# Optimization experiments

Measured on AMD Instinct MI355X. Metric: run time of the kernel, lower is better.

Reference implementation:

```python
import jax, jax.numpy as jnp
import numpy as np

N, B, S, E, D, L, H, OUT = 16384, 32, 512, 262144, 256, 4, 4, 768
DH = D // H
ATOM_VOCABS = [119, 9, 12, 12, 10, 6, 9, 2, 2]
BOND_VOCABS = [22, 6, 2]
BN_EPS = 1e-5


def bn(x, g, b):
    # BatchNorm1d over nodes (training-mode statistics, deterministic)
    mu = x.mean(0)
    var = ((x - mu) ** 2).mean(0)
    return (x - mu) * jax.lax.rsqrt(var + BN_EPS) * g + b


def setup_inputs():
    key = jax.random.key(0)
    ks = iter(jax.random.split(key, 80))
    x = jnp.stack([jax.random.randint(next(ks), (N,), 0, v) for v in ATOM_VOCABS], 1)
    edge_attr = jnp.stack([jax.random.randint(next(ks), (E,), 0, v) for v in BOND_VOCABS], 1)
    epg = E // B  # edges per graph, edges stay within their graph
    gid = jnp.arange(E) // epg
    src = jax.random.randint(next(ks), (E,), 0, S) + gid * S
    dst = jax.random.randint(next(ks), (E,), 0, S) + gid * S
    edge_index = jnp.stack([src, dst], 0)
    batch_vec = jnp.arange(N) // S  # B equal-sized graphs, contiguous

    def rn(shape, std=0.02):
        return jax.random.normal(next(ks), shape, jnp.float32) * std

    inp = dict(x=x, edge_attr=edge_attr, edge_index=edge_index, batch_vec=batch_vec)
    inp['atom_tab'] = rn((len(ATOM_VOCABS), max(ATOM_VOCABS), D))
    inp['bond_tab'] = rn((len(BOND_VOCABS), max(BOND_VOCABS), D))
    inp['elin_w'] = rn((L, D, D)); inp['elin_b'] = jnp.zeros((L, D))
    inp['eps'] = jnp.zeros((L,))  # GINE train_eps init 0
    inp['gw1'] = rn((L, D, 2 * D)); inp['gb1'] = jnp.zeros((L, 2 * D))
    inp['gw2'] = rn((L, 2 * D, D)); inp['gb2'] = jnp.zeros((L, D))
    inp['aw_in'] = rn((L, D, 3 * D)); inp['ab_in'] = jnp.zeros((L, 3 * D))
    inp['aw_out'] = rn((L, D, D)); inp['ab_out'] = jnp.zeros((L, D))
    for n in ('n1', 'n2', 'n3'):
        inp[n + 'g'] = jnp.ones((L, D)); inp[n + 'b'] = jnp.zeros((L, D))
    inp['mw1'] = rn((L, D, 2 * D)); inp['mb1'] = jnp.zeros((L, 2 * D))
    inp['mw2'] = rn((L, 2 * D, D)); inp['mb2'] = jnp.zeros((L, D))
    inp['pw1'] = rn((D, D)); inp['pb1'] = jnp.zeros((D,))
    inp['pw2'] = rn((D, OUT)); inp['pb2'] = jnp.zeros((OUT,))
    return inp


def forward(x, edge_attr, edge_index, batch_vec, atom_tab, bond_tab, elin_w, elin_b, eps,
            gw1, gb1, gw2, gb2, aw_in, ab_in, aw_out, ab_out,
            n1g, n1b, n2g, n2b, n3g, n3b, mw1, mb1, mw2, mb2,
            pw1, pb1, pw2, pb2):
    # AtomEncoder / BondEncoder: sum of per-feature embeddings
    h = atom_tab[jnp.arange(atom_tab.shape[0])[None, :], x].sum(1)      # [N, D]
    e = bond_tab[jnp.arange(bond_tab.shape[0])[None, :], edge_attr].sum(1)  # [E, D]
    src, dst = edge_index[0], edge_index[1]
    scale = 1.0 / np.sqrt(DH)
    for l in range(L):
        # --- GINEConv local branch ---
        el = e @ elin_w[l] + elin_b[l]                       # edge lin
        msg = jax.nn.relu(h[src] + el)                       # [E, D]
        agg = jax.ops.segment_sum(msg, dst, num_segments=N)  # scatter-add
        hc = (1.0 + eps[l]) * h + agg
        hc = jax.nn.relu(hc @ gw1[l] + gb1[l]) @ gw2[l] + gb2[l]
        hc = bn(hc + h, n1g[l], n1b[l])
        # --- global multihead attention (dense per-graph batch, all slots valid) ---
        hd = h.reshape(B, S, D)
        qkv = hd @ aw_in[l] + ab_in[l]
        q, k, v = jnp.split(qkv, 3, axis=-1)
        q = q.reshape(B, S, H, DH).transpose(0, 2, 1, 3)
        k = k.reshape(B, S, H, DH).transpose(0, 2, 1, 3)
        v = v.reshape(B, S, H, DH).transpose(0, 2, 1, 3)
        attn = jax.nn.softmax(jnp.einsum('bhqd,bhkd->bhqk', q, k) * scale, axis=-1)
        ao = jnp.einsum('bhqk,bhkd->bhqd', attn, v).transpose(0, 2, 1, 3).reshape(N, D)
        ao = ao @ aw_out[l] + ab_out[l]
        ha = bn(ao + h, n2g[l], n2b[l])
        # --- combine + MLP ---
        out = hc + ha
        out = out + (jax.nn.relu(out @ mw1[l] + mb1[l]) @ mw2[l] + mb2[l])
        h = bn(out, n3g[l], n3b[l])
    # global mean pool
    counts = jax.ops.segment_sum(jnp.ones((N, 1), h.dtype), batch_vec, num_segments=B)
    g = jax.ops.segment_sum(h, batch_vec, num_segments=B) / counts
    z = jax.nn.relu(g @ pw1 + pb1) @ pw2 + pb2
    return z / jnp.linalg.norm(z, axis=-1, keepdims=True)


def reference(x, edge_attr, edge_index, batch_vec, atom_tab, bond_tab, elin_w, elin_b, eps,
              gw1, gb1, gw2, gb2, aw_in, ab_in, aw_out, ab_out,
              n1g, n1b, n2g, n2b, n3g, n3b, mw1, mb1, mw2, mb2,
              pw1, pb1, pw2, pb2):
    return forward(x, edge_attr, edge_index, batch_vec, atom_tab, bond_tab, elin_w, elin_b, eps,
                   gw1, gb1, gw2, gb2, aw_in, ab_in, aw_out, ab_out,
                   n1g, n1b, n2g, n2b, n3g, n3b, mw1, mb1, mw2, mb2,
                   pw1, pb1, pw2, pb2)
```

## Files before the change

kernel.cpp:

```cpp
#include <hip/hip_runtime.h>
#include <hip/hip_bf16.h>
#include <math.h>

#define N_NODES 16384
#define NB      32
#define S_PG    512
#define NE      262144
#define EPG     8192
#define D       256
#define D2      512
#define D3      768
#define NL      4
#define NH      4
#define DHD     64
#define OUTD    768
#define NCOMBO  264
#define WT_PER_LAYER 786432

typedef short s8v __attribute__((ext_vector_type(8)));
typedef float f4v __attribute__((ext_vector_type(4)));

__device__ __forceinline__ unsigned bfr(float f) {
    unsigned u = __float_as_uint(f);
    return (u + 0x7fffu + ((u >> 16) & 1u)) >> 16;
}
__device__ __forceinline__ float b2f(unsigned short u) {
    return __uint_as_float(((unsigned)u) << 16);
}

__global__ __launch_bounds__(256) void k_atom_enc(const int* __restrict__ x,
                                                  const float* __restrict__ tab,
                                                  float* __restrict__ h,
                                                  unsigned short* __restrict__ hb) {
    int node = blockIdx.x * 4 + (threadIdx.x >> 6);
    int lane = threadIdx.x & 63;
    int dd = lane << 2;
    float4 acc = {0.f, 0.f, 0.f, 0.f};
#pragma unroll
    for (int f = 0; f < 9; ++f) {
        int v = x[node * 9 + f];
        const float4 t = *(const float4*)&tab[((size_t)(f * 119 + v)) * D + dd];
        acc.x += t.x; acc.y += t.y; acc.z += t.z; acc.w += t.w;
    }
    *(float4*)&h[(size_t)node * D + dd] = acc;
    ushort4 o;
    o.x = (unsigned short)bfr(acc.x); o.y = (unsigned short)bfr(acc.y);
    o.z = (unsigned short)bfr(acc.z); o.w = (unsigned short)bfr(acc.w);
    *(ushort4*)&hb[(size_t)node * D + dd] = o;
}

__global__ __launch_bounds__(256) void k_bondw(const float* __restrict__ bond_tab,
                                               const float* __restrict__ elin_w,
                                               float* __restrict__ bw) {
    int blk = blockIdx.x;
    int l = blk / 66, fv = blk % 66;
    int dout = threadIdx.x;
    const float* tabrow = bond_tab + (size_t)fv * D;
    const float* w = elin_w + (size_t)l * D * D;
    float acc = 0.f;
    for (int d = 0; d < D; ++d) acc = fmaf(tabrow[d], w[d * D + dout], acc);
    bw[((size_t)l * 66 + fv) * D + dout] = acc;
}

__global__ __launch_bounds__(256) void k_combo(const float* __restrict__ bw,
                                               const float* __restrict__ elin_b,
                                               unsigned short* __restrict__ ctb) {
    int b = blockIdx.x;
    int l = b / NCOMBO, cid = b % NCOMBO;
    int a0 = cid / 12, a1 = (cid % 12) / 2, a2 = cid & 1;
    int d = threadIdx.x;
    const float* bwl = bw + (size_t)l * 66 * D;
    float v = bwl[(size_t)a0 * D + d] + bwl[(size_t)(22 + a1) * D + d] +
              bwl[(size_t)(44 + a2) * D + d] + elin_b[(size_t)l * D + d];
    ctb[((size_t)l * NCOMBO + cid) * D + d] = (unsigned short)bfr(v);
}

__global__ __launch_bounds__(256) void k_zero16k(int* __restrict__ p) {
    p[blockIdx.x * 256 + threadIdx.x] = 0;
}
__global__ __launch_bounds__(256) void k_zero_stats(float* __restrict__ p) {
    for (int i = 0; i < 6; ++i) p[i * 256 + threadIdx.x] = 0.f;
}
__global__ __launch_bounds__(256) void k_hist(const int* __restrict__ dst, int* __restrict__ deg) {
    int e = blockIdx.x * 256 + threadIdx.x;
    atomicAdd(&deg[dst[e]], 1);
}
__global__ __launch_bounds__(256) void k_scan(const int* __restrict__ deg,
                                              int* __restrict__ row_ptr,
                                              int* __restrict__ cursor) {
    __shared__ int partial[256];
    int t = threadIdx.x;
    int base = t * 64;
    int s = 0;
    for (int i = 0; i < 64; ++i) s += deg[base + i];
    partial[t] = s;
    __syncthreads();
    for (int dstp = 1; dstp < 256; dstp <<= 1) {
        int v = (t >= dstp) ? partial[t - dstp] : 0;
        __syncthreads();
        partial[t] += v;
        __syncthreads();
    }
    int run = partial[t] - s;
    for (int i = 0; i < 64; ++i) {
        int dcur = deg[base + i];
        row_ptr[base + i] = run;
        cursor[base + i] = run;
        run += dcur;
    }
    if (t == 255) row_ptr[N_NODES] = run;
}
__global__ __launch_bounds__(256) void k_scatter(const int* __restrict__ src,
                                                 const int* __restrict__ dst,
                                                 const int* __restrict__ ea,
                                                 int* __restrict__ cursor,
                                                 int2* __restrict__ sorted) {
    int e = blockIdx.x * 256 + threadIdx.x;
    int d = dst[e];
    int pos = atomicAdd(&cursor[d], 1);
    int cid = ea[e * 3] * 12 + ea[e * 3 + 1] * 2 + ea[e * 3 + 2];
    sorted[pos] = make_int2(src[e], cid);
}

__global__ __launch_bounds__(256) void k_gine_agg(const unsigned short* __restrict__ hb,
                                                  const float* __restrict__ h,
                                                  const unsigned short* __restrict__ ctb,
                                                  const float* __restrict__ eps, int l,
                                                  const int* __restrict__ row_ptr,
                                                  const int2* __restrict__ sorted,
                                                  unsigned short* __restrict__ aggb) {
    int w = threadIdx.x >> 6;
    int lane = threadIdx.x & 63;
    int n = blockIdx.x * 4 + w;
    int dd = lane << 2;
    int beg = row_ptr[n], end = row_ptr[n + 1];
    float4 acc = {0.f, 0.f, 0.f, 0.f};
    int i = beg;
    for (; i + 2 <= end; i += 2) {
        int2 e0 = sorted[i];
        int2 e1 = sorted[i + 1];
        ushort4 h0 = *(const ushort4*)&hb[(size_t)e0.x * D + dd];
        ushort4 c0 = *(const ushort4*)&ctb[(size_t)e0.y * D + dd];
        ushort4 h1 = *(const ushort4*)&hb[(size_t)e1.x * D + dd];
        ushort4 c1 = *(const ushort4*)&ctb[(size_t)e1.y * D + dd];
        acc.x += fmaxf(b2f(h0.x) + b2f(c0.x), 0.f) + fmaxf(b2f(h1.x) + b2f(c1.x), 0.f);
        acc.y += fmaxf(b2f(h0.y) + b2f(c0.y), 0.f) + fmaxf(b2f(h1.y) + b2f(c1.y), 0.f);
        acc.z += fmaxf(b2f(h0.z) + b2f(c0.z), 0.f) + fmaxf(b2f(h1.z) + b2f(c1.z), 0.f);
        acc.w += fmaxf(b2f(h0.w) + b2f(c0.w), 0.f) + fmaxf(b2f(h1.w) + b2f(c1.w), 0.f);
    }
    if (i < end) {
        int2 e0 = sorted[i];
        ushort4 h0 = *(const ushort4*)&hb[(size_t)e0.x * D + dd];
        ushort4 c0 = *(const ushort4*)&ctb[(size_t)e0.y * D + dd];
        acc.x += fmaxf(b2f(h0.x) + b2f(c0.x), 0.f);
        acc.y += fmaxf(b2f(h0.y) + b2f(c0.y), 0.f);
        acc.z += fmaxf(b2f(h0.z) + b2f(c0.z), 0.f);
        acc.w += fmaxf(b2f(h0.w) + b2f(c0.w), 0.f);
    }
    float s1p = 1.f + eps[l];
    float4 hn = *(const float4*)&h[(size_t)n * D + dd];
    ushort4 o;
    o.x = (unsigned short)bfr(s1p * hn.x + acc.x);
    o.y = (unsigned short)bfr(s1p * hn.y + acc.y);
    o.z = (unsigned short)bfr(s1p * hn.z + acc.z);
    o.w = (unsigned short)bfr(s1p * hn.w + acc.w);
    *(ushort4*)&aggb[(size_t)n * D + dd] = o;
}

__global__ __launch_bounds__(256) void k_wcvt(const float* __restrict__ gw1, const float* __restrict__ gw2,
                                              const float* __restrict__ aw_in, const float* __restrict__ aw_out,
                                              const float* __restrict__ mw1, const float* __restrict__ mw2,
                                              unsigned short* __restrict__ WT) {
    const int KS[6]   = {256, 512, 256, 256, 256, 512};
    const int NS[6]   = {512, 256, 768, 256, 512, 256};
    const int TOFF[7] = {0, 128, 256, 448, 512, 640, 768};
    const int DOFF[6] = {0, 131072, 262144, 458752, 524288, 655360};
    int b = blockIdx.x;
    int l = b / 768, wb = b % 768;
    int widx = 0;
    while (wb >= TOFF[widx + 1]) ++widx;
    int t = wb - TOFF[widx];
    int K = KS[widx], N = NS[widx];
    int nn = N / 32;
    int kt = t / nn, nt = t % nn;
    const float* srcs[6] = {gw1, gw2, aw_in, aw_out, mw1, mw2};
    const float* W = srcs[widx] + (size_t)l * K * N;
    unsigned short* WTp = WT + (size_t)l * WT_PER_LAYER + DOFF[widx];
    __shared__ float tile[32][33];
    int tid = threadIdx.x;
    int r = tid >> 3, c4 = (tid & 7) << 2;
    float4 v = *(const float4*)&W[(size_t)(kt * 32 + r) * N + nt * 32 + c4];
    tile[r][c4] = v.x; tile[r][c4 + 1] = v.y; tile[r][c4 + 2] = v.z; tile[r][c4 + 3] = v.w;
    __syncthreads();
    int nr = tid >> 3, kc = (tid & 7) << 2;
    ushort4 o;
    o.x = (unsigned short)bfr(tile[kc + 0][nr]);
    o.y = (unsigned short)bfr(tile[kc + 1][nr]);
    o.z = (unsigned short)bfr(tile[kc + 2][nr]);
    o.w = (unsigned short)bfr(tile[kc + 3][nr]);
    *(ushort4*)&WTp[(size_t)(nt * 32 + nr) * K + kt * 32 + kc] = o;
}

template<int RELU, int RES, int OBF, int STAT>
__global__ __launch_bounds__(256) void k_mm2(const unsigned short* __restrict__ A,
                                             const unsigned short* __restrict__ BT,
                                             const float* __restrict__ bias,
                                             const float* __restrict__ res,
                                             void* __restrict__ Cp,
                                             float* __restrict__ stat,
                                             int M, int N, int K) {
    __shared__ unsigned short As[128 * 64];
    __shared__ unsigned short Bs[128 * 64];
    const int tid = threadIdx.x;
    const int row0 = blockIdx.y * 128, col0 = blockIdx.x * 128;
    const int w = tid >> 6, l = tid & 63;
    const int wm = w >> 1, wn = w & 1;
    const int lr = l & 15, lq = l >> 4;
    const int srow = l >> 3;
    const int scol = (l & 7) * 8;
    f4v acc[4][4] = {};

    const unsigned short* Ag = A + (size_t)(row0 + w * 32 + srow) * K + scol;
    const unsigned short* Bg = BT + (size_t)(col0 + w * 32 + srow) * K + scol;
    unsigned short* Al = &As[(w * 32) * 64];
    unsigned short* Bl = &Bs[(w * 32) * 64];

    for (int k0 = 0; k0 < K; k0 += 64) {
#pragma unroll
        for (int it = 0; it < 4; ++it) {
            __builtin_amdgcn_global_load_lds(
                (const __attribute__((address_space(1))) unsigned*)(Ag + (size_t)(it * 8) * K + k0),
                (__attribute__((address_space(3))) unsigned*)(Al + it * 8 * 64), 16, 0, 0);
            __builtin_amdgcn_global_load_lds(
                (const __attribute__((address_space(1))) unsigned*)(Bg + (size_t)(it * 8) * K + k0),
                (__attribute__((address_space(3))) unsigned*)(Bl + it * 8 * 64), 16, 0, 0);
        }
        asm volatile("s_waitcnt vmcnt(0)" ::: "memory");
        __syncthreads();
#pragma unroll
        for (int kk = 0; kk < 2; ++kk) {
            s8v af[4], bf[4];
#pragma unroll
            for (int m = 0; m < 4; ++m)
                af[m] = *(const s8v*)&As[(wm * 64 + m * 16 + lr) * 64 + kk * 32 + lq * 8];
#pragma unroll
            for (int n = 0; n < 4; ++n)
                bf[n] = *(const s8v*)&Bs[(wn * 64 + n * 16 + lr) * 64 + kk * 32 + lq * 8];
#pragma unroll
            for (int m = 0; m < 4; ++m)
#pragma unroll
                for (int n = 0; n < 4; ++n)
                    acc[m][n] = __builtin_amdgcn_mfma_f32_16x16x32_bf16(af[m], bf[n], acc[m][n], 0, 0, 0);
        }
        __syncthreads();
    }
    float cs[4], cs2[4];
#pragma unroll
    for (int n = 0; n < 4; ++n) { cs[n] = 0.f; cs2[n] = 0.f; }
#pragma unroll
    for (int n = 0; n < 4; ++n) {
        int c = col0 + wn * 64 + n * 16 + lr;
        float bv = bias[c];
#pragma unroll
        for (int m = 0; m < 4; ++m) {
#pragma unroll
            for (int j = 0; j < 4; ++j) {
                int r = row0 + wm * 64 + m * 16 + lq * 4 + j;
                float v = acc[m][n][j] + bv;
                if (RES) v += res[(size_t)r * N + c];
                if (STAT) { cs[n] += v; cs2[n] += v * v; }
                if (RELU) v = fmaxf(v, 0.f);
                if (OBF) ((unsigned short*)Cp)[(size_t)r * N + c] = (unsigned short)bfr(v);
                else ((float*)Cp)[(size_t)r * N + c] = v;
            }
        }
    }
    if (STAT) {
#pragma unroll
        for (int n = 0; n < 4; ++n) {
            float s = cs[n], s2 = cs2[n];
            s += __shfl_xor(s, 16);  s2 += __shfl_xor(s2, 16);
            s += __shfl_xor(s, 32);  s2 += __shfl_xor(s2, 32);
            if (lq == 0) {
                int c = col0 + wn * 64 + n * 16 + lr;
                atomicAdd(&stat[c], s);
                atomicAdd(&stat[256 + c], s2);
            }
        }
    }
}

__global__ __launch_bounds__(256) void k_bn_finish(float* __restrict__ acc,
                                                   float* __restrict__ ms) {
    int c = threadIdx.x;
    float s = acc[c], s2 = acc[256 + c];
    float mean = s / (float)N_NODES;
    float var = s2 / (float)N_NODES - mean * mean;
    ms[c] = mean;
    ms[D + c] = rsqrtf(var + 1e-5f);
    acc[c] = 0.f;
    acc[256 + c] = 0.f;
}

__global__ __launch_bounds__(256) void k_bn12(const float* __restrict__ t1,
                                              const float* __restrict__ ms1,
                                              const float* __restrict__ g1,
                                              const float* __restrict__ b1,
                                              const float* __restrict__ t2,
                                              const float* __restrict__ ms2,
                                              const float* __restrict__ g2,
                                              const float* __restrict__ b2,
                                              float* __restrict__ y,
                                              unsigned short* __restrict__ yb) {
    size_t i4 = (size_t)blockIdx.x * blockDim.x + threadIdx.x;
    int c = (int)((i4 & 63) << 2);
    float4 v1 = ((const float4*)t1)[i4];
    float4 v2 = ((const float4*)t2)[i4];
    float4 v;
    v.x = (v1.x - ms1[c + 0]) * ms1[D + c + 0] * g1[c + 0] + b1[c + 0]
        + (v2.x - ms2[c + 0]) * ms2[D + c + 0] * g2[c + 0] + b2[c + 0];
    v.y = (v1.y - ms1[c + 1]) * ms1[D + c + 1] * g1[c + 1] + b1[c + 1]
        + (v2.y - ms2[c + 1]) * ms2[D + c + 1] * g2[c + 1] + b2[c + 1];
    v.z = (v1.z - ms1[c + 2]) * ms1[D + c + 2] * g1[c + 2] + b1[c + 2]
        + (v2.z - ms2[c + 2]) * ms2[D + c + 2] * g2[c + 2] + b2[c + 2];
    v.w = (v1.w - ms1[c + 3]) * ms1[D + c + 3] * g1[c + 3] + b1[c + 3]
        + (v2.w - ms2[c + 3]) * ms2[D + c + 3] * g2[c + 3] + b2[c + 3];
    ((float4*)y)[i4] = v;
    ushort4 o;
    o.x = (unsigned short)bfr(v.x); o.y = (unsigned short)bfr(v.y);
    o.z = (unsigned short)bfr(v.z); o.w = (unsigned short)bfr(v.w);
    ((ushort4*)yb)[i4] = o;
}

__global__ __launch_bounds__(256) void k_bn_apply(const float* __restrict__ x,
                                                  const float* __restrict__ ms,
                                                  const float* __restrict__ g,
                                                  const float* __restrict__ b,
                                                  float* __restrict__ y,
                                                  unsigned short* __restrict__ yb) {
    size_t i4 = (size_t)blockIdx.x * blockDim.x + threadIdx.x;
    int c = (int)((i4 & 63) << 2);
    float4 v = ((const float4*)x)[i4];
    v.x = (v.x - ms[c + 0]) * ms[D + c + 0] * g[c + 0] + b[c + 0];
    v.y = (v.y - ms[c + 1]) * ms[D + c + 1] * g[c + 1] + b[c + 1];
    v.z = (v.z - ms[c + 2]) * ms[D + c + 2] * g[c + 2] + b[c + 2];
    v.w = (v.w - ms[c + 3]) * ms[D + c + 3] * g[c + 3] + b[c + 3];
    ((float4*)y)[i4] = v;
    ushort4 o;
    o.x = (unsigned short)bfr(v.x); o.y = (unsigned short)bfr(v.y);
    o.z = (unsigned short)bfr(v.z); o.w = (unsigned short)bfr(v.w);
    ((ushort4*)yb)[i4] = o;
}

__global__ __launch_bounds__(256) void k_flash_mfma(const unsigned short* __restrict__ qkv,
                                                    unsigned short* __restrict__ ao) {
    __shared__ unsigned short Ks[64][72];
    __shared__ unsigned short VT[64][66];
    __shared__ unsigned short Ps[4][16][72];
    const int bh = blockIdx.x;
    const int b = bh >> 2, hh = bh & 3;
    const int i0 = blockIdx.y << 6;
    const int tid = threadIdx.x;
    const int w = tid >> 6, l = tid & 63;
    const int lr = l & 15, lq = l >> 4;
    const int hd = hh * DHD;
    const size_t rowbase = (size_t)(b * S_PG) * D3;

    s8v aq[2];
    {
        const unsigned short* qrow = &qkv[rowbase + (size_t)(i0 + w * 16 + lr) * D3 + hd + lq * 8];
        aq[0] = *(const s8v*)&qrow[0];
        aq[1] = *(const s8v*)&qrow[32];
    }

    float mrow[4] = {-INFINITY, -INFINITY, -INFINITY, -INFINITY};
    float lrow[4] = {0.f, 0.f, 0.f, 0.f};
    f4v oacc[4] = {};

    const int skv = tid >> 2;
    const int sd0 = (tid & 3) << 4;

    for (int j0 = 0; j0 < S_PG; j0 += 64) {
        __syncthreads();
        {
            const unsigned short* kr = &qkv[rowbase + (size_t)(j0 + skv) * D3 + D + hd + sd0];
            *(uint4*)&Ks[skv][sd0]     = *(const uint4*)&kr[0];
            *(uint4*)&Ks[skv][sd0 + 8] = *(const uint4*)&kr[8];
            const unsigned short* vr = &qkv[rowbase + (size_t)(j0 + skv) * D3 + D2 + hd + sd0];
            unsigned short vv[16];
            *(uint4*)&vv[0] = *(const uint4*)&vr[0];
            *(uint4*)&vv[8] = *(const uint4*)&vr[8];
#pragma unroll
            for (int i = 0; i < 16; ++i) VT[sd0 + i][skv] = vv[i];
        }
        __syncthreads();
        f4v sc[4] = {};
#pragma unroll
        for (int nt = 0; nt < 4; ++nt) {
            s8v bk0 = *(const s8v*)&Ks[nt * 16 + lr][lq * 8];
            s8v bk1 = *(const s8v*)&Ks[nt * 16 + lr][32 + lq * 8];
            sc[nt] = __builtin_amdgcn_mfma_f32_16x16x32_bf16(aq[0], bk0, sc[nt], 0, 0, 0);
            sc[nt] = __builtin_amdgcn_mfma_f32_16x16x32_bf16(aq[1], bk1, sc[nt], 0, 0, 0);
        }
        float ps[4][4], alpha[4];
#pragma unroll
        for (int j = 0; j < 4; ++j) {
#pragma unroll
            for (int nt = 0; nt < 4; ++nt) ps[nt][j] = sc[nt][j] * 0.125f;
            float pm = fmaxf(fmaxf(ps[0][j], ps[1][j]), fmaxf(ps[2][j], ps[3][j]));
#pragma unroll
            for (int off = 1; off < 16; off <<= 1) pm = fmaxf(pm, __shfl_xor(pm, off));
            float mn = fmaxf(mrow[j], pm);
            alpha[j] = __expf(mrow[j] - mn);
            float rs = 0.f;
#pragma unroll
            for (int nt = 0; nt < 4; ++nt) { ps[nt][j] = __expf(ps[nt][j] - mn); rs += ps[nt][j]; }
#pragma unroll
            for (int off = 1; off < 16; off <<= 1) rs += __shfl_xor(rs, off);
            lrow[j] = lrow[j] * alpha[j] + rs;
            mrow[j] = mn;
        }
#pragma unroll
        for (int nt = 0; nt < 4; ++nt)
#pragma unroll
            for (int j = 0; j < 4; ++j)
                Ps[w][lq * 4 + j][nt * 16 + lr] = (unsigned short)bfr(ps[nt][j]);
#pragma unroll
        for (int ntd = 0; ntd < 4; ++ntd)
#pragma unroll
            for (int j = 0; j < 4; ++j) oacc[ntd][j] *= alpha[j];
        s8v pa0 = *(const s8v*)&Ps[w][lr][lq * 8];
        s8v pa1 = *(const s8v*)&Ps[w][lr][32 + lq * 8];
#pragma unroll
        for (int ntd = 0; ntd < 4; ++ntd) {
            s8v bv0 = *(const s8v*)&VT[ntd * 16 + lr][lq * 8];
            s8v bv1 = *(const s8v*)&VT[ntd * 16 + lr][32 + lq * 8];
            oacc[ntd] = __builtin_amdgcn_mfma_f32_16x16x32_bf16(pa0, bv0, oacc[ntd], 0, 0, 0);
            oacc[ntd] = __builtin_amdgcn_mfma_f32_16x16x32_bf16(pa1, bv1, oacc[ntd], 0, 0, 0);
        }
    }
#pragma unroll
    for (int j = 0; j < 4; ++j) {
        float inv = 1.f / lrow[j];
        int node = b * S_PG + i0 + w * 16 + lq * 4 + j;
#pragma unroll
        for (int ntd = 0; ntd < 4; ++ntd)
            ao[(size_t)node * D + hd + ntd * 16 + lr] = (unsigned short)bfr(oacc[ntd][j] * inv);
    }
}

__global__ __launch_bounds__(256) void k_pool(const float* __restrict__ h, float* __restrict__ g) {
    int b = blockIdx.x, c = threadIdx.x;
    const float* p = h + (size_t)b * S_PG * D + c;
    float s = 0.f;
    for (int r = 0; r < S_PG; ++r) s += p[(size_t)r * D];
    g[b * D + c] = s * (1.f / (float)S_PG);
}

__global__ __launch_bounds__(256) void k_final(const float* __restrict__ g,
                                               const float* __restrict__ pw1,
                                               const float* __restrict__ pb1,
                                               const float* __restrict__ pw2,
                                               const float* __restrict__ pb2,
                                               float* __restrict__ out) {
    __shared__ float gs[D];
    __shared__ float ts[D];
    __shared__ float red[4];
    int b = blockIdx.x, tid = threadIdx.x;
    gs[tid] = g[b * D + tid];
    __syncthreads();
    float acc = pb1[tid];
    for (int d = 0; d < D; ++d) acc = fmaf(gs[d], pw1[d * D + tid], acc);
    ts[tid] = fmaxf(acc, 0.f);
    __syncthreads();
    float z[3];
#pragma unroll
    for (int rep = 0; rep < 3; ++rep) {
        int j = tid + rep * 256;
        float a = pb2[j];
        for (int d = 0; d < D; ++d) a = fmaf(ts[d], pw2[(size_t)d * OUTD + j], a);
        z[rep] = a;
    }
    float ss = z[0] * z[0] + z[1] * z[1] + z[2] * z[2];
#pragma unroll
    for (int o = 32; o >= 1; o >>= 1) ss += __shfl_xor(ss, o);
    if ((tid & 63) == 0) red[tid >> 6] = ss;
    __syncthreads();
    float rn = rsqrtf(red[0] + red[1] + red[2] + red[3]);
#pragma unroll
    for (int rep = 0; rep < 3; ++rep) out[b * OUTD + tid + rep * 256] = z[rep] * rn;
}

extern "C" void kernel_launch(void* const* d_in, const int* in_sizes, int n_in,
                              void* d_out, int out_size, void* d_ws, size_t ws_size,
                              hipStream_t stream) {
    const int* x        = (const int*)d_in[0];
    const int* ea       = (const int*)d_in[1];
    const int* eidx     = (const int*)d_in[2];
    const float* atom_tab = (const float*)d_in[4];
    const float* bond_tab = (const float*)d_in[5];
    const float* elin_w = (const float*)d_in[6];
    const float* elin_b = (const float*)d_in[7];
    const float* eps    = (const float*)d_in[8];
    const float* gw1    = (const float*)d_in[9];
    const float* gb1    = (const float*)d_in[10];
    const float* gw2    = (const float*)d_in[11];
    const float* gb2    = (const float*)d_in[12];
    const float* aw_in  = (const float*)d_in[13];
    const float* ab_in  = (const float*)d_in[14];
    const float* aw_out = (const float*)d_in[15];
    const float* ab_out = (const float*)d_in[16];
    const float* n1g    = (const float*)d_in[17];
    const float* n1b    = (const float*)d_in[18];
    const float* n2g    = (const float*)d_in[19];
    const float* n2b    = (const float*)d_in[20];
    const float* n3g    = (const float*)d_in[21];
    const float* n3b    = (const float*)d_in[22];
    const float* mw1    = (const float*)d_in[23];
    const float* mb1    = (const float*)d_in[24];
    const float* mw2    = (const float*)d_in[25];
    const float* mb2    = (const float*)d_in[26];
    const float* pw1    = (const float*)d_in[27];
    const float* pb1    = (const float*)d_in[28];
    const float* pw2    = (const float*)d_in[29];
    const float* pb2    = (const float*)d_in[30];

    char* ws = (char*)d_ws;
    size_t off = 0;
    auto alloc = [&](size_t bytes) {
        void* p = ws + off;
        off += (bytes + 255) & ~(size_t)255;
        return p;
    };
    float*  h    = (float*)alloc((size_t)N_NODES * D * 4);
    float*  bufB = (float*)alloc((size_t)N_NODES * D * 4);
    float*  tmp1 = (float*)alloc((size_t)N_NODES * D * 4);
    unsigned short* hb = (unsigned short*)alloc((size_t)N_NODES * D * 2);
    char*   U    = (char*)alloc((size_t)N_NODES * D3 * 2);
    unsigned short* bfA = (unsigned short*)alloc((size_t)N_NODES * D3 * 2);
    unsigned short* WT  = (unsigned short*)alloc((size_t)NL * WT_PER_LAYER * 2);
    float*  bw   = (float*)alloc((size_t)NL * 66 * D * 4);
    unsigned short* ctb = (unsigned short*)alloc((size_t)NL * NCOMBO * D * 2);
    int*    deg  = (int*)alloc((size_t)N_NODES * 4);
    int*    row_ptr = (int*)alloc((size_t)(N_NODES + 1) * 4);
    int*    cursor  = (int*)alloc((size_t)N_NODES * 4);
    int2*   sorted  = (int2*)alloc((size_t)NE * 8);
    float*  statacc = (float*)alloc((size_t)3 * 512 * 4);
    float*  msbuf   = (float*)alloc((size_t)3 * 2 * D * 4);
    float*  g    = (float*)alloc((size_t)NB * D * 4);
    (void)ws_size; (void)in_sizes; (void)n_in; (void)out_size;

    float* tmp23 = (float*)U;
    unsigned short* qkv = (unsigned short*)U;
    unsigned short* aggb  = bfA;
    unsigned short* ao    = bfA;
    unsigned short* bufBb = bfA;
    unsigned short* hid   = bfA + (size_t)N_NODES * D;
    float* ms1 = msbuf, *ms2 = msbuf + 2 * D, *ms3 = msbuf + 4 * D;

    const int* srcp = eidx;
    const int* dstp = eidx + NE;
    const int EW = N_NODES * D / 1024;

    k_zero16k<<<N_NODES / 256, 256, 0, stream>>>(deg);
    k_zero_stats<<<1, 256, 0, stream>>>(statacc);
    k_hist<<<NE / 256, 256, 0, stream>>>(dstp, deg);
    k_scan<<<1, 256, 0, stream>>>(deg, row_ptr, cursor);
    k_scatter<<<NE / 256, 256, 0, stream>>>(srcp, dstp, ea, cursor, sorted);
    k_atom_enc<<<N_NODES / 4, 256, 0, stream>>>(x, atom_tab, h, hb);
    k_bondw<<<NL * 66, 256, 0, stream>>>(bond_tab, elin_w, bw);
    k_combo<<<NL * NCOMBO, 256, 0, stream>>>(bw, elin_b, ctb);
    k_wcvt<<<NL * 768, 256, 0, stream>>>(gw1, gw2, aw_in, aw_out, mw1, mw2, WT);

    for (int l = 0; l < NL; ++l) {
        const unsigned short* WTl = WT + (size_t)l * WT_PER_LAYER;
        k_gine_agg<<<N_NODES / 4, 256, 0, stream>>>(hb, h, ctb + (size_t)l * NCOMBO * D, eps, l,
                                                    row_ptr, sorted, aggb);
        k_mm2<1, 0, 1, 0><<<dim3(D2 / 128, N_NODES / 128), 256, 0, stream>>>(
            aggb, WTl + 0, gb1 + (size_t)l * D2, nullptr, hid, nullptr, N_NODES, D2, D);
        k_mm2<0, 1, 0, 1><<<dim3(D / 128, N_NODES / 128), 256, 0, stream>>>(
            hid, WTl + 131072, gb2 + (size_t)l * D, h, tmp1, statacc, N_NODES, D, D2);
        k_bn_finish<<<1, 256, 0, stream>>>(statacc, ms1);
        k_mm2<0, 0, 1, 0><<<dim3(D3 / 128, N_NODES / 128), 256, 0, stream>>>(
            hb, WTl + 262144, ab_in + (size_t)l * D3, nullptr, qkv, nullptr, N_NODES, D3, D);
        k_flash_mfma<<<dim3(NB * NH, S_PG / 64), 256, 0, stream>>>(qkv, ao);
        k_mm2<0, 1, 0, 1><<<dim3(D / 128, N_NODES / 128), 256, 0, stream>>>(
            ao, WTl + 458752, ab_out + (size_t)l * D, h, tmp23, statacc + 512, N_NODES, D, D);
        k_bn_finish<<<1, 256, 0, stream>>>(statacc + 512, ms2);
        k_bn12<<<EW, 256, 0, stream>>>(tmp1, ms1, n1g + l * D, n1b + l * D,
                                       tmp23, ms2, n2g + l * D, n2b + l * D, bufB, bufBb);
        k_mm2<1, 0, 1, 0><<<dim3(D2 / 128, N_NODES / 128), 256, 0, stream>>>(
            bufBb, WTl + 524288, mb1 + (size_t)l * D2, nullptr, hid, nullptr, N_NODES, D2, D);
        k_mm2<0, 1, 0, 1><<<dim3(D / 128, N_NODES / 128), 256, 0, stream>>>(
            hid, WTl + 655360, mb2 + (size_t)l * D, bufB, tmp23, statacc + 1024, N_NODES, D, D2);
        k_bn_finish<<<1, 256, 0, stream>>>(statacc + 1024, ms3);
        k_bn_apply<<<EW, 256, 0, stream>>>(tmp23, ms3, n3g + l * D, n3b + l * D, h, hb);
    }
    k_pool<<<NB, 256, 0, stream>>>(h, g);
    k_final<<<NB, 256, 0, stream>>>(g, pw1, pb1, pw2, pb2, (float*)d_out);
}
```

Before: 1.009 ms.

## Fuse GINE and QKV GEMMs, use 64-row tiles for narrow GEMMs, merge BN finish

New measurement: 942.9 us. 1.07x faster.

```diff
diff --git a/kernel.cpp b/kernel.cpp
--- a/kernel.cpp
+++ b/kernel.cpp
@@ -290,6 +290,171 @@
     }
 }
 
+__global__ __launch_bounds__(256) void k_mm2_dual(const unsigned short* __restrict__ A1,
+                                                  const unsigned short* __restrict__ B1,
+                                                  const float* __restrict__ bias1,
+                                                  unsigned short* __restrict__ C1, int N1, int nb1,
+                                                  const unsigned short* __restrict__ A2,
+                                                  const unsigned short* __restrict__ B2,
+                                                  const float* __restrict__ bias2,
+                                                  unsigned short* __restrict__ C2, int N2,
+                                                  int K) {
+    __shared__ unsigned short As[128 * 64];
+    __shared__ unsigned short Bs[128 * 64];
+    const unsigned short* A; const unsigned short* BT; const float* bias;
+    unsigned short* C; int N, cb, relu;
+    if ((int)blockIdx.x < nb1) { A = A1; BT = B1; bias = bias1; C = C1; N = N1; cb = blockIdx.x; relu = 1; }
+    else { A = A2; BT = B2; bias = bias2; C = C2; N = N2; cb = blockIdx.x - nb1; relu = 0; }
+    const int tid = threadIdx.x;
+    const int row0 = blockIdx.y * 128, col0 = cb * 128;
+    const int w = tid >> 6, l = tid & 63;
+    const int wm = w >> 1, wn = w & 1;
+    const int lr = l & 15, lq = l >> 4;
+    const int srow = l >> 3;
+    const int scol = (l & 7) * 8;
+    f4v acc[4][4] = {};
+
+    const unsigned short* Ag = A + (size_t)(row0 + w * 32 + srow) * K + scol;
+    const unsigned short* Bg = BT + (size_t)(col0 + w * 32 + srow) * K + scol;
+    unsigned short* Al = &As[(w * 32) * 64];
+    unsigned short* Bl = &Bs[(w * 32) * 64];
+
+    for (int k0 = 0; k0 < K; k0 += 64) {
+#pragma unroll
+        for (int it = 0; it < 4; ++it) {
+            __builtin_amdgcn_global_load_lds(
+                (const __attribute__((address_space(1))) unsigned*)(Ag + (size_t)(it * 8) * K + k0),
+                (__attribute__((address_space(3))) unsigned*)(Al + it * 8 * 64), 16, 0, 0);
+            __builtin_amdgcn_global_load_lds(
+                (const __attribute__((address_space(1))) unsigned*)(Bg + (size_t)(it * 8) * K + k0),
+                (__attribute__((address_space(3))) unsigned*)(Bl + it * 8 * 64), 16, 0, 0);
+        }
+        asm volatile("s_waitcnt vmcnt(0)" ::: "memory");
+        __syncthreads();
+#pragma unroll
+        for (int kk = 0; kk < 2; ++kk) {
+            s8v af[4], bf[4];
+#pragma unroll
+            for (int m = 0; m < 4; ++m)
+                af[m] = *(const s8v*)&As[(wm * 64 + m * 16 + lr) * 64 + kk * 32 + lq * 8];
+#pragma unroll
+            for (int n = 0; n < 4; ++n)
+                bf[n] = *(const s8v*)&Bs[(wn * 64 + n * 16 + lr) * 64 + kk * 32 + lq * 8];
+#pragma unroll
+            for (int m = 0; m < 4; ++m)
+#pragma unroll
+                for (int n = 0; n < 4; ++n)
+                    acc[m][n] = __builtin_amdgcn_mfma_f32_16x16x32_bf16(af[m], bf[n], acc[m][n], 0, 0, 0);
+        }
+        __syncthreads();
+    }
+#pragma unroll
+    for (int n = 0; n < 4; ++n) {
+        int c = col0 + wn * 64 + n * 16 + lr;
+        float bv = bias[c];
+#pragma unroll
+        for (int m = 0; m < 4; ++m) {
+#pragma unroll
+            for (int j = 0; j < 4; ++j) {
+                int r = row0 + wm * 64 + m * 16 + lq * 4 + j;
+                float v = acc[m][n][j] + bv;
+                if (relu) v = fmaxf(v, 0.f);
+                C[(size_t)r * N + c] = (unsigned short)bfr(v);
+            }
+        }
+    }
+}
+
+template<int RELU, int RES, int OBF, int STAT>
+__global__ __launch_bounds__(256) void k_mm64(const unsigned short* __restrict__ A,
+                                              const unsigned short* __restrict__ BT,
+                                              const float* __restrict__ bias,
+                                              const float* __restrict__ res,
+                                              void* __restrict__ Cp,
+                                              float* __restrict__ stat,
+                                              int M, int N, int K) {
+    __shared__ unsigned short As[64 * 64];
+    __shared__ unsigned short Bs[128 * 64];
+    const int tid = threadIdx.x;
+    const int row0 = blockIdx.y * 64, col0 = blockIdx.x * 128;
+    const int w = tid >> 6, l = tid & 63;
+    const int wn = w;
+    const int lr = l & 15, lq = l >> 4;
+    const int srow = l >> 3;
+    const int scol = (l & 7) * 8;
+    f4v acc[4][2] = {};
+
+    const unsigned short* Ag = A + (size_t)(row0 + w * 16 + srow) * K + scol;
+    const unsigned short* Bg = BT + (size_t)(col0 + w * 32 + srow) * K + scol;
+    unsigned short* Al = &As[(w * 16) * 64];
+    unsigned short* Bl = &Bs[(w * 32) * 64];
+
+    for (int k0 = 0; k0 < K; k0 += 64) {
+#pragma unroll
+        for (int it = 0; it < 2; ++it)
+            __builtin_amdgcn_global_load_lds(
+                (const __attribute__((address_space(1))) unsigned*)(Ag + (size_t)(it * 8) * K + k0),
+                (__attribute__((address_space(3))) unsigned*)(Al + it * 8 * 64), 16, 0, 0);
+#pragma unroll
+        for (int it = 0; it < 4; ++it)
+            __builtin_amdgcn_global_load_lds(
+                (const __attribute__((address_space(1))) unsigned*)(Bg + (size_t)(it * 8) * K + k0),
+                (__attribute__((address_space(3))) unsigned*)(Bl + it * 8 * 64), 16, 0, 0);
+        asm volatile("s_waitcnt vmcnt(0)" ::: "memory");
+        __syncthreads();
+#pragma unroll
+        for (int kk = 0; kk < 2; ++kk) {
+            s8v af[4], bf[2];
+#pragma unroll
+            for (int m = 0; m < 4; ++m)
+                af[m] = *(const s8v*)&As[(m * 16 + lr) * 64 + kk * 32 + lq * 8];
+#pragma unroll
+            for (int n = 0; n < 2; ++n)
+                bf[n] = *(const s8v*)&Bs[(wn * 32 + n * 16 + lr) * 64 + kk * 32 + lq * 8];
+#pragma unroll
+            for (int m = 0; m < 4; ++m)
+#pragma unroll
+                for (int n = 0; n < 2; ++n)
+                    acc[m][n] = __builtin_amdgcn_mfma_f32_16x16x32_bf16(af[m], bf[n], acc[m][n], 0, 0, 0);
+        }
+        __syncthreads();
+    }
+    float cs[2], cs2[2];
+#pragma unroll
+    for (int n = 0; n < 2; ++n) { cs[n] = 0.f; cs2[n] = 0.f; }
+#pragma unroll
+    for (int n = 0; n < 2; ++n) {
+        int c = col0 + wn * 32 + n * 16 + lr;
+        float bv = bias[c];
+#pragma unroll
+        for (int m = 0; m < 4; ++m) {
+#pragma unroll
+            for (int j = 0; j < 4; ++j) {
+                int r = row0 + m * 16 + lq * 4 + j;
+                float v = acc[m][n][j] + bv;
+                if (RES) v += res[(size_t)r * N + c];
+                if (STAT) { cs[n] += v; cs2[n] += v * v; }
+                if (RELU) v = fmaxf(v, 0.f);
+                if (OBF) ((unsigned short*)Cp)[(size_t)r * N + c] = (unsigned short)bfr(v);
+                else ((float*)Cp)[(size_t)r * N + c] = v;
+            }
+        }
+    }
+    if (STAT) {
+#pragma unroll
+        for (int n = 0; n < 2; ++n) {
+            float s = cs[n], s2 = cs2[n];
+            s += __shfl_xor(s, 16);  s2 += __shfl_xor(s2, 16);
+            s += __shfl_xor(s, 32);  s2 += __shfl_xor(s2, 32);
+            if (lq == 0) {
+                int c = col0 + wn * 32 + n * 16 + lr;
+                atomicAdd(&stat[c], s);
+                atomicAdd(&stat[256 + c], s2);
+            }
+        }
+    }
+}
+
 __global__ __launch_bounds__(256) void k_bn_finish(float* __restrict__ acc,
                                                    float* __restrict__ ms) {
     int c = threadIdx.x;
@@ -300,6 +465,20 @@
     ms[D + c] = rsqrtf(var + 1e-5f);
     acc[c] = 0.f;
     acc[256 + c] = 0.f;
+}
+__global__ __launch_bounds__(256) void k_bn_finish2(float* __restrict__ acc,
+                                                    float* __restrict__ ms) {
+    int s0 = blockIdx.x;
+    float* a = acc + (size_t)s0 * 512;
+    float* m = ms + (size_t)s0 * 2 * D;
+    int c = threadIdx.x;
+    float s = a[c], s2 = a[256 + c];
+    float mean = s / (float)N_NODES;
+    float var = s2 / (float)N_NODES - mean * mean;
+    m[c] = mean;
+    m[D + c] = rsqrtf(var + 1e-5f);
+    a[c] = 0.f;
+    a[256 + c] = 0.f;
 }
 
 __global__ __launch_bounds__(256) void k_bn12(const float* __restrict__ t1,
@@ -355,7 +534,7 @@
 __global__ __launch_bounds__(256) void k_flash_mfma(const unsigned short* __restrict__ qkv,
                                                     unsigned short* __restrict__ ao) {
     __shared__ unsigned short Ks[64][72];
-    __shared__ unsigned short VT[64][66];
+    __shared__ unsigned short VT[64][72];
     __shared__ unsigned short Ps[4][16][72];
     const int bh = blockIdx.x;
     const int b = bh >> 2, hh = bh & 3;
@@ -379,6 +558,8 @@
 
     const int skv = tid >> 2;
     const int sd0 = (tid & 3) << 4;
+    const int d0v = (tid >> 4) << 2;
+    const int kv0 = (tid & 15) << 2;
 
     for (int j0 = 0; j0 < S_PG; j0 += 64) {
         __syncthreads();
@@ -386,12 +567,21 @@
             const unsigned short* kr = &qkv[rowbase + (size_t)(j0 + skv) * D3 + D + hd + sd0];
             *(uint4*)&Ks[skv][sd0]     = *(const uint4*)&kr[0];
             *(uint4*)&Ks[skv][sd0 + 8] = *(const uint4*)&kr[8];
-            const unsigned short* vr = &qkv[rowbase + (size_t)(j0 + skv) * D3 + D2 + hd + sd0];
-            unsigned short vv[16];
-            *(uint4*)&vv[0] = *(const uint4*)&vr[0];
-            *(uint4*)&vv[8] = *(const uint4*)&vr[8];
-#pragma unroll
-            for (int i = 0; i < 16; ++i) VT[sd0 + i][skv] = vv[i];
+            unsigned short vv[4][4];
+#pragma unroll
+            for (int i = 0; i < 4; ++i) {
+                uint2 lv = *(const uint2*)&qkv[rowbase + (size_t)(j0 + kv0 + i) * D3 + D2 + hd + d0v];
+                vv[i][0] = (unsigned short)(lv.x & 0xffffu);
+                vv[i][1] = (unsigned short)(lv.x >> 16);
+                vv[i][2] = (unsigned short)(lv.y & 0xffffu);
+                vv[i][3] = (unsigned short)(lv.y >> 16);
+            }
+#pragma unroll
+            for (int i2 = 0; i2 < 4; ++i2) {
+                ushort4 o4;
+                o4.x = vv[0][i2]; o4.y = vv[1][i2]; o4.z = vv[2][i2]; o4.w = vv[3][i2];
+                *(ushort4*)&VT[d0v + i2][kv0] = o4;
+            }
         }
         __syncthreads();
         f4v sc[4] = {};
@@ -556,7 +746,7 @@
     unsigned short* ao    = bfA;
     unsigned short* bufBb = bfA;
     unsigned short* hid   = bfA + (size_t)N_NODES * D;
-    float* ms1 = msbuf, *ms2 = msbuf + 2 * D, *ms3 = msbuf + 4 * D;
+    float* ms1 = msbuf, *ms3 = msbuf + 4 * D;
 
     const int* srcp = eidx;
     const int* dstp = eidx + NE;
@@ -576,22 +766,20 @@
         const unsigned short* WTl = WT + (size_t)l * WT_PER_LAYER;
         k_gine_agg<<<N_NODES / 4, 256, 0, stream>>>(hb, h, ctb + (size_t)l * NCOMBO * D, eps, l,
                                                     row_ptr, sorted, aggb);
-        k_mm2<1, 0, 1, 0><<<dim3(D2 / 128, N_NODES / 128), 256, 0, stream>>>(
-            aggb, WTl + 0, gb1 + (size_t)l * D2, nullptr, hid, nullptr, N_NODES, D2, D);
-        k_mm2<0, 1, 0, 1><<<dim3(D / 128, N_NODES / 128), 256, 0, stream>>>(
+        k_mm2_dual<<<dim3(10, N_NODES / 128), 256, 0, stream>>>(
+            aggb, WTl + 0, gb1 + (size_t)l * D2, hid, D2, 4,
+            hb, WTl + 262144, ab_in + (size_t)l * D3, qkv, D3, D);
+        k_mm64<0, 1, 0, 1><<<dim3(D / 128, N_NODES / 64), 256, 0, stream>>>(
             hid, WTl + 131072, gb2 + (size_t)l * D, h, tmp1, statacc, N_NODES, D, D2);
-        k_bn_finish<<<1, 256, 0, stream>>>(statacc, ms1);
-        k_mm2<0, 0, 1, 0><<<dim3(D3 / 128, N_NODES / 128), 256, 0, stream>>>(
-            hb, WTl + 262144, ab_in + (size_t)l * D3, nullptr, qkv, nullptr, N_NODES, D3, D);
         k_flash_mfma<<<dim3(NB * NH, S_PG / 64), 256, 0, stream>>>(qkv, ao);
-        k_mm2<0, 1, 0, 1><<<dim3(D / 128, N_NODES / 128), 256, 0, stream>>>(
+        k_mm64<0, 1, 0, 1><<<dim3(D / 128, N_NODES / 64), 256, 0, stream>>>(
             ao, WTl + 458752, ab_out + (size_t)l * D, h, tmp23, statacc + 512, N_NODES, D, D);
-        k_bn_finish<<<1, 256, 0, stream>>>(statacc + 512, ms2);
+        k_bn_finish2<<<2, 256, 0, stream>>>(statacc, msbuf);
         k_bn12<<<EW, 256, 0, stream>>>(tmp1, ms1, n1g + l * D, n1b + l * D,
-                                       tmp23, ms2, n2g + l * D, n2b + l * D, bufB, bufBb);
+                                       tmp23, msbuf + 2 * D, n2g + l * D, n2b + l * D, bufB, bufBb);
         k_mm2<1, 0, 1, 0><<<dim3(D2 / 128, N_NODES / 128), 256, 0, stream>>>(
             bufBb, WTl + 524288, mb1 + (size_t)l * D2, nullptr, hid, nullptr, N_NODES, D2, D);
-        k_mm2<0, 1, 0, 1><<<dim3(D / 128, N_NODES / 128), 256, 0, stream>>>(
+        k_mm64<0, 1, 0, 1><<<dim3(D / 128, N_NODES / 64), 256, 0, stream>>>(
             hid, WTl + 655360, mb2 + (size_t)l * D, bufB, tmp23, statacc + 1024, N_NODES, D, D2);
         k_bn_finish<<<1, 256, 0, stream>>>(statacc + 1024, ms3);
         k_bn_apply<<<EW, 256, 0, stream>>>(tmp23, ms3, n3g + l * D, n3b + l * D, h, hb);
```
